# Kernel tuning notes

Measured on AMD Instinct MI355X. Metric: run time of the kernel, lower is better.

Reference implementation:

```python
import jax, jax.numpy as jnp
import numpy as np

N_NODES = 102600
T = 64             # timesteps looped over by the LSTMCell
F_IN = 5           # LSTMCell input size
H = 64             # hidden / GAT channel dim
N_EDGES = 16 * N_NODES


def setup_inputs() -> dict:
    key = jax.random.key(0)
    ks = jax.random.split(key, 12)
    s = 0.1
    return {
        "x": jax.random.normal(ks[0], (N_NODES, T, F_IN), jnp.float32),
        "W_ih": jax.random.normal(ks[1], (4 * H, F_IN), jnp.float32) * s,
        "W_hh": jax.random.normal(ks[2], (4 * H, H), jnp.float32) * s,
        "b_ih": jax.random.normal(ks[3], (4 * H,), jnp.float32) * s,
        "b_hh": jax.random.normal(ks[4], (4 * H,), jnp.float32) * s,
        "gat_w": jax.random.normal(ks[5], (H, H), jnp.float32) * s,
        "att_src": jax.random.normal(ks[6], (H,), jnp.float32) * s,
        "att_dst": jax.random.normal(ks[7], (H,), jnp.float32) * s,
        "gat_bias": jax.random.normal(ks[8], (H,), jnp.float32) * s,
        "fc_w": jax.random.normal(ks[9], (1, H), jnp.float32) * s,
        "fc_b": jax.random.normal(ks[10], (1,), jnp.float32) * s,
        "edge_index": jax.random.randint(ks[11], (2, N_EDGES), 0, N_NODES, dtype=jnp.int64),
    }


def reference(x, W_ih, W_hh, b_ih, b_hh, gat_w, att_src, att_dst, gat_bias, fc_w, fc_b, edge_index):
    N = x.shape[0]
    h0 = jnp.zeros((N, H), x.dtype)
    c0 = jnp.zeros((N, H), x.dtype)

    # --- per-timestep LSTMCell recurrence (torch gate order: i, f, g, o) ---
    def step(carry, xt):
        h, c = carry
        gates = xt @ W_ih.T + b_ih + h @ W_hh.T + b_hh  # [N, 4H]
        i, f, g, o = jnp.split(gates, 4, axis=-1)
        c = jax.nn.sigmoid(f) * c + jax.nn.sigmoid(i) * jnp.tanh(g)
        h = jax.nn.sigmoid(o) * jnp.tanh(c)
        return (h, c), None

    (h, _), _ = jax.lax.scan(step, (h0, c0), jnp.swapaxes(x, 0, 1))  # scan over T

    # --- GATConv(64, 64), heads=1, add_self_loops=True, negative_slope=0.2 ---
    xp = h @ gat_w.T                                   # [N, H] transformed features
    loops = jnp.arange(N, dtype=edge_index.dtype)
    src = jnp.concatenate([edge_index[0], loops])      # message source j
    dst = jnp.concatenate([edge_index[1], loops])      # message target i
    a_src = xp @ att_src                               # [N]
    a_dst = xp @ att_dst                               # [N]
    alpha = jax.nn.leaky_relu(a_src[src] + a_dst[dst], 0.2)  # [E+N]
    # segment softmax over incoming edges per dst node
    amax = jax.ops.segment_max(alpha, dst, num_segments=N)
    ae = jnp.exp(alpha - amax[dst])
    denom = jax.ops.segment_sum(ae, dst, num_segments=N)
    ae = ae / denom[dst]
    out = jax.ops.segment_sum(ae[:, None] * xp[src], dst, num_segments=N) + gat_bias

    # --- fc: Linear(64, 1) + LeakyReLU (default slope 0.01) ---
    return jax.nn.leaky_relu(out @ fc_w.T + fc_b, 0.01)
```

## Files before the change

kernel.cpp:

```cpp
#include <hip/hip_runtime.h>
#include <cstdint>
#include <cstddef>

#define T_STEPS 64
#define F_INP 5
#define LOG2E 1.44269504088896340736f

typedef _Float16 f16x8 __attribute__((ext_vector_type(8)));
typedef float f32x4 __attribute__((ext_vector_type(4)));

__device__ __forceinline__ float leaky(float x, float s){ return x>0.f? x : s*x; }
__device__ __forceinline__ float rcpf(float x){ return __builtin_amdgcn_rcpf(x); }
__device__ __forceinline__ float exp2fast(float x){ return __builtin_amdgcn_exp2f(x); }

__global__ __launch_bounds__(256, 4) void lstm_mfma(
    const float* __restrict__ x, const float* __restrict__ W_ih,
    const float* __restrict__ W_hh, const float* __restrict__ b_ih,
    const float* __restrict__ b_hh, float* __restrict__ h_out, int N)
{
  __shared__ __align__(16) _Float16 Hs0[32][64];
  __shared__ __align__(16) _Float16 Hs1[32][64];
  __shared__ __align__(16) _Float16 Xs0[32][8];
  __shared__ __align__(16) _Float16 Xs1[32][8];
  __shared__ __align__(16) _Float16 Zero8[8];

  const int tid   = threadIdx.x;
  const int lane  = tid & 63;
  const int wq    = tid >> 6;
  const int col16 = lane & 15;
  const int grp   = lane >> 4;
  const int base  = blockIdx.x * 32;

  f16x8 Bh[4][2], Bx[4];
  #pragma unroll
  for (int n=0;n<4;n++){
    const float sc = (n==2) ? 2.f*LOG2E : LOG2E;
    const int gate = n*64 + wq*16 + col16;
    #pragma unroll
    for (int kk=0;kk<2;kk++){
      const float* p = W_hh + gate*64 + kk*32 + grp*8;
      #pragma unroll
      for (int e=0;e<8;e++) Bh[n][kk][e] = (_Float16)(p[e]*sc);
    }
    f16x8 bx = {0,0,0,0,0,0,0,0};
    if (grp==0){
      #pragma unroll
      for (int e=0;e<5;e++) bx[e] = (_Float16)(W_ih[gate*5+e]*sc);
      bx[5] = (_Float16)((b_ih[gate]+b_hh[gate])*sc);
    }
    Bx[n] = bx;
  }

  ((float4*)&Hs0[0][0])[tid] = float4{0.f,0.f,0.f,0.f};
  if (tid==0) ((float4*)Zero8)[0] = float4{0.f,0.f,0.f,0.f};

  const int xnode = tid;
  const bool xown = (tid < 32);
  const int gxn = base + xnode;
  if (xown){
    f16x8 xh = {0,0,0,0,0,0,0,0}; xh[5] = (_Float16)1.f;
    if (gxn < N){
      const float* xp_ = x + (size_t)gxn*(T_STEPS*F_INP);
      #pragma unroll
      for (int j=0;j<F_INP;j++) xh[j] = (_Float16)xp_[j];
    }
    *(f16x8*)&Xs0[xnode][0] = xh;
  }

  const int sw = (col16&7)<<3;
  int roff0[2], roff1[2], xoffm[2], soff[2][4];
  const int j = wq*16 + col16;
  #pragma unroll
  for (int m=0;m<2;m++){
    const int nodeA = 16*m + col16;
    roff0[m] = nodeA*64 + ((grp*8) ^ sw);
    roff1[m] = nodeA*64 + ((32 + grp*8) ^ sw);
    xoffm[m] = nodeA*8;
    #pragma unroll
    for (int r=0;r<4;r++){
      const int node = 16*m + 4*grp + r;
      soff[m][r] = node*64 + (j ^ ((4*(grp&1)+r)<<3));
    }
  }

  float creg[2][4];
  #pragma unroll
  for (int m=0;m<2;m++)
    #pragma unroll
    for (int r=0;r<4;r++) creg[m][r]=0.f;

  __syncthreads();

#define LSTM_STEP(HC, HN, XC, XN, T, LAST) {                                   \
    float xf0=0.f,xf1=0.f,xf2=0.f,xf3=0.f,xf4=0.f;                             \
    const bool xload = (!(LAST)) && xown && (gxn < N);                         \
    if (xload){                                                                \
      const float* xp_ = x + (size_t)gxn*(T_STEPS*F_INP) + ((T)+1)*F_INP;      \
      xf0=xp_[0];xf1=xp_[1];xf2=xp_[2];xf3=xp_[3];xf4=xp_[4];                  \
    }                                                                          \
    _Pragma("unroll")                                                          \
    for (int m=0;m<2;m++){                                                     \
      f16x8 a0 = *(const f16x8*)(&HC[0][0] + roff0[m]);                        \
      f16x8 a1 = *(const f16x8*)(&HC[0][0] + roff1[m]);                        \
      const _Float16* px = (grp==0) ? (&XC[0][0] + xoffm[m]) : Zero8;          \
      f16x8 ax = *(const f16x8*)px;                                            \
      f32x4 z4 = f32x4{0.f,0.f,0.f,0.f};                                       \
      f32x4 ac0=z4, ac1=z4, ac2=z4, ac3=z4;                                    \
      ac0 = __builtin_amdgcn_mfma_f32_16x16x32_f16(a0, Bh[0][0], ac0, 0,0,0);  \
      ac1 = __builtin_amdgcn_mfma_f32_16x16x32_f16(a0, Bh[1][0], ac1, 0,0,0);  \
      ac2 = __builtin_amdgcn_mfma_f32_16x16x32_f16(a0, Bh[2][0], ac2, 0,0,0);  \
      ac3 = __builtin_amdgcn_mfma_f32_16x16x32_f16(a0, Bh[3][0], ac3, 0,0,0);  \
      ac0 = __builtin_amdgcn_mfma_f32_16x16x32_f16(a1, Bh[0][1], ac0, 0,0,0);  \
      ac1 = __builtin_amdgcn_mfma_f32_16x16x32_f16(a1, Bh[1][1], ac1, 0,0,0);  \
      ac2 = __builtin_amdgcn_mfma_f32_16x16x32_f16(a1, Bh[2][1], ac2, 0,0,0);  \
      ac3 = __builtin_amdgcn_mfma_f32_16x16x32_f16(a1, Bh[3][1], ac3, 0,0,0);  \
      ac0 = __builtin_amdgcn_mfma_f32_16x16x32_f16(ax, Bx[0],    ac0, 0,0,0);  \
      ac1 = __builtin_amdgcn_mfma_f32_16x16x32_f16(ax, Bx[1],    ac1, 0,0,0);  \
      ac2 = __builtin_amdgcn_mfma_f32_16x16x32_f16(ax, Bx[2],    ac2, 0,0,0);  \
      ac3 = __builtin_amdgcn_mfma_f32_16x16x32_f16(ax, Bx[3],    ac3, 0,0,0);  \
      _Pragma("unroll")                                                        \
      for (int r=0;r<4;r++){                                                   \
        float e_i = exp2fast(-ac0[r]);                                         \
        float e_f = exp2fast(-ac1[r]);                                         \
        float zg2 = fminf(ac2[r], 60.f);                                       \
        float e_g = exp2fast(zg2);                                             \
        float e_o = exp2fast(-ac3[r]);                                         \
        float Ag = (1.f+e_i)*(1.f+e_g);                                        \
        float Bf = 1.f+e_f;                                                    \
        float rD = rcpf(Ag*Bf);                                                \
        float cn = (creg[m][r]*Ag + (e_g-1.f)*Bf)*rD;                          \
        creg[m][r] = cn;                                                       \
        float c2 = fminf(cn*(2.f*LOG2E), 120.f);                               \
        float e_c = exp2fast(c2);                                              \
        float hv = (e_c-1.f)*rcpf((1.f+e_o)*(1.f+e_c));                        \
        if (LAST){                                                             \
          const int gn = base + 16*m + 4*grp + r;                              \
          if (gn < N) h_out[(size_t)gn*64 + j] = hv;                           \
        } else {                                                               \
          (&HN[0][0])[soff[m][r]] = (_Float16)hv;                              \
        }                                                                      \
      }                                                                        \
    }                                                                          \
    if (!(LAST) && xown){                                                      \
      f16x8 xh = {0,0,0,0,0,0,0,0}; xh[5] = (_Float16)1.f;                     \
      if (xload){                                                              \
        xh[0]=(_Float16)xf0; xh[1]=(_Float16)xf1; xh[2]=(_Float16)xf2;         \
        xh[3]=(_Float16)xf3; xh[4]=(_Float16)xf4;                              \
      }                                                                        \
      *(f16x8*)&XN[xnode][0] = xh;                                             \
    }                                                                          \
  }

  for (int tt=0; tt<T_STEPS/2; ++tt){
    LSTM_STEP(Hs0, Hs1, Xs0, Xs1, 2*tt, false);
    __syncthreads();
    LSTM_STEP(Hs1, Hs0, Xs1, Xs0, 2*tt+1, (tt==T_STEPS/2-1));
    __syncthreads();
  }
#undef LSTM_STEP
}

__global__ void gat_setup(const int* __restrict__ ei,
                          const float* __restrict__ gat_w,
                          const float* __restrict__ att_src,
                          const float* __restrict__ att_dst,
                          const float* __restrict__ fc_w,
                          const float* __restrict__ gat_bias,
                          const float* __restrict__ fc_b,
                          float* __restrict__ vcomb,
                          unsigned* __restrict__ mode)
{
  int j = threadIdx.x;
  unsigned long long nz = __ballot(ei[2*j+1] != 0);
  float bdp = gat_bias[j]*fc_w[j];
  #pragma unroll
  for (int off=32; off; off>>=1) bdp += __shfl_down(bdp, off);
  if (j==0){
    *mode = (nz==0ULL) ? 1u : 0u;
    vcomb[192] = bdp + fc_b[0];
  }
  float va=0.f, vd=0.f, vf=0.f;
  #pragma unroll 8
  for (int k=0;k<64;k++){
    float g = gat_w[k*64+j];
    va += att_src[k]*g;
    vd += att_dst[k]*g;
    vf += fc_w[k]*g;
  }
  vcomb[j]=va; vcomb[64+j]=vd; vcomb[128+j]=vf;
}

__global__ __launch_bounds__(256) void gat_prep(
    const float* __restrict__ h_in, const float* __restrict__ vcomb,
    float* __restrict__ a_src, float* __restrict__ a_dst,
    float* __restrict__ xfv, float* __restrict__ denom,
    float* __restrict__ oacc, int N)
{
  int n = blockIdx.x*256 + threadIdx.x;
  if (n>=N) return;
  const float4* hp = (const float4*)(h_in + (size_t)n*64);
  const float4* va = (const float4*)vcomb;
  const float4* vd = (const float4*)(vcomb+64);
  const float4* vf = (const float4*)(vcomb+128);
  float as=0.f, ad=0.f, xf=0.f;
  #pragma unroll
  for (int q=0;q<16;q++){
    float4 h = hp[q], a = va[q], d = vd[q], f = vf[q];
    as += a.x*h.x + a.y*h.y + a.z*h.z + a.w*h.w;
    ad += d.x*h.x + d.y*h.y + d.z*h.z + d.w*h.w;
    xf += f.x*h.x + f.y*h.y + f.z*h.z + f.w*h.w;
  }
  a_src[n]=as; a_dst[n]=ad; xfv[n]=xf;
  denom[n]=0.f; oacc[n]=0.f;
}

__device__ __forceinline__ void load_edge(const int* ei, unsigned mode,
                                          long long e, long long E,
                                          int& s, int& d)
{
  if (e>=E){ s=d=(int)(e-E); }
  else if (mode){
    const long long* e64 = (const long long*)ei;
    s=(int)e64[e]; d=(int)e64[E+e];
  } else {
    s=ei[e]; d=ei[E+e];
  }
}

__global__ __launch_bounds__(256) void edge_pass(
    const int* __restrict__ ei, const unsigned* __restrict__ mode_p,
    const float* __restrict__ a_src, const float* __restrict__ a_dst,
    const float* __restrict__ xfv,
    float* __restrict__ denom, float* __restrict__ oacc,
    long long E, long long total)
{
  long long e = (long long)blockIdx.x*256 + threadIdx.x;
  if (e>=total) return;
  int s,d;
  load_edge(ei, *mode_p, e, E, s, d);
  float al = leaky(a_src[s]+a_dst[d], 0.2f);
  float ew = __expf(al);
  atomicAdd(&denom[d], ew);
  atomicAdd(&oacc[d], ew * xfv[s]);
}

__global__ __launch_bounds__(256) void finalize(
    const float* __restrict__ oacc, const float* __restrict__ denom,
    const float* __restrict__ vcomb, float* __restrict__ out, int N)
{
  int n = blockIdx.x*256+threadIdx.x;
  if (n>=N) return;
  float v = oacc[n] * rcpf(denom[n]) + vcomb[192];
  out[n] = leaky(v, 0.01f);
}

extern "C" void kernel_launch(void* const* d_in, const int* in_sizes, int n_in,
                              void* d_out, int out_size, void* d_ws, size_t ws_size,
                              hipStream_t stream)
{
  const float* x      = (const float*)d_in[0];
  const float* W_ih   = (const float*)d_in[1];
  const float* W_hh   = (const float*)d_in[2];
  const float* b_ih   = (const float*)d_in[3];
  const float* b_hh   = (const float*)d_in[4];
  const float* gat_w  = (const float*)d_in[5];
  const float* att_s  = (const float*)d_in[6];
  const float* att_d  = (const float*)d_in[7];
  const float* gat_b  = (const float*)d_in[8];
  const float* fc_w   = (const float*)d_in[9];
  const float* fc_b   = (const float*)d_in[10];
  const int*   ei     = (const int*)d_in[11];

  const int N = in_sizes[0]/(T_STEPS*F_INP);
  const long long E = in_sizes[11]/2;
  const long long total = E + N;

  float* ws = (float*)d_ws;
  size_t off = 0;
  float* h_out   = ws + off; off += (size_t)N*64;
  float* a_src   = ws + off; off += (size_t)N;
  float* a_dst   = ws + off; off += (size_t)N;
  float* xfv     = ws + off; off += (size_t)N;
  float* denom   = ws + off; off += (size_t)N;
  float* oacc    = ws + off; off += (size_t)N;
  float* vcomb   = ws + off; off += 256;
  unsigned* mode = (unsigned*)(ws + off); off += 1;

  gat_setup<<<1,64,0,stream>>>(ei, gat_w, att_s, att_d, fc_w, gat_b, fc_b, vcomb, mode);

  lstm_mfma<<<dim3((N+31)/32), dim3(256), 0, stream>>>(
      x, W_ih, W_hh, b_ih, b_hh, h_out, N);

  gat_prep<<<dim3((N+255)/256), dim3(256), 0, stream>>>(
      h_out, vcomb, a_src, a_dst, xfv, denom, oacc, N);

  int eb = (int)((total+255)/256);
  edge_pass<<<dim3(eb), dim3(256), 0, stream>>>(ei, mode, a_src, a_dst, xfv, denom, oacc, E, total);

  finalize<<<dim3((N+255)/256), dim3(256), 0, stream>>>(oacc, denom, vcomb, (float*)d_out, N);
}
```

Measured before the change: 661.4 us.

## Fuse GAT projection into LSTM epilogue and pack src scores

Computes the per-node attention and fc projections directly from the final hidden state held in shared memory at the end of the LSTM kernel. This removes the gat_prep launch and the N x 64 float h_out round trip through global memory. The x loads are now spread across 160 threads with one scalar each, replacing 32 threads loading five values. The MFMA batches for both row halves are issued before the gate math, and a_src and xfv are packed into one float2 so each edge needs one gather for them instead of two. The costs are extra shared memory (a 32x65 float buffer), which may reduce occupancy, and higher register pressure from holding both sets of accumulators.

```diff
diff --git a/kernel.cpp b/kernel.cpp
--- a/kernel.cpp
+++ b/kernel.cpp
@@ -16,13 +16,16 @@
 __global__ __launch_bounds__(256, 4) void lstm_mfma(
     const float* __restrict__ x, const float* __restrict__ W_ih,
     const float* __restrict__ W_hh, const float* __restrict__ b_ih,
-    const float* __restrict__ b_hh, float* __restrict__ h_out, int N)
+    const float* __restrict__ b_hh, const float* __restrict__ vcomb,
+    float2* __restrict__ asx, float* __restrict__ a_dst,
+    float* __restrict__ denom, float* __restrict__ oacc, int N)
 {
   __shared__ __align__(16) _Float16 Hs0[32][64];
   __shared__ __align__(16) _Float16 Hs1[32][64];
   __shared__ __align__(16) _Float16 Xs0[32][8];
   __shared__ __align__(16) _Float16 Xs1[32][8];
   __shared__ __align__(16) _Float16 Zero8[8];
+  __shared__ __align__(16) float    Hf[32][65];
 
   const int tid   = threadIdx.x;
   const int lane  = tid & 63;
@@ -54,17 +57,18 @@
   ((float4*)&Hs0[0][0])[tid] = float4{0.f,0.f,0.f,0.f};
   if (tid==0) ((float4*)Zero8)[0] = float4{0.f,0.f,0.f,0.f};
 
-  const int xnode = tid;
-  const bool xown = (tid < 32);
-  const int gxn = base + xnode;
-  if (xown){
-    f16x8 xh = {0,0,0,0,0,0,0,0}; xh[5] = (_Float16)1.f;
-    if (gxn < N){
-      const float* xp_ = x + (size_t)gxn*(T_STEPS*F_INP);
-      #pragma unroll
-      for (int j=0;j<F_INP;j++) xh[j] = (_Float16)xp_[j];
-    }
-    *(f16x8*)&Xs0[xnode][0] = xh;
+  const int  xn5  = tid/5, xe5 = tid - xn5*5;
+  const bool xact = (tid < 160);
+  const int  gxnode = base + xn5;
+  const bool xlive  = xact && (gxnode < N);
+  const float* xptr = x + (size_t)(xlive ? gxnode : 0)*(T_STEPS*F_INP) + xe5 + F_INP;
+  if (xact){
+    float v0 = xlive ? x[(size_t)gxnode*(T_STEPS*F_INP) + xe5] : 0.f;
+    Xs0[xn5][xe5] = (_Float16)v0;
+  }
+  if (tid < 32){
+    Xs0[tid][5]=(_Float16)1.f; Xs0[tid][6]=(_Float16)0.f; Xs0[tid][7]=(_Float16)0.f;
+    Xs1[tid][5]=(_Float16)1.f; Xs1[tid][6]=(_Float16)0.f; Xs1[tid][7]=(_Float16)0.f;
   }
 
   const int sw = (col16&7)<<3;
@@ -91,13 +95,10 @@
 
   __syncthreads();
 
-#define LSTM_STEP(HC, HN, XC, XN, T, LAST) {                                   \
-    float xf0=0.f,xf1=0.f,xf2=0.f,xf3=0.f,xf4=0.f;                             \
-    const bool xload = (!(LAST)) && xown && (gxn < N);                         \
-    if (xload){                                                                \
-      const float* xp_ = x + (size_t)gxn*(T_STEPS*F_INP) + ((T)+1)*F_INP;      \
-      xf0=xp_[0];xf1=xp_[1];xf2=xp_[2];xf3=xp_[3];xf4=xp_[4];                  \
-    }                                                                          \
+#define LSTM_STEP(HC, HN, XC, XN, XOFF, LAST) {                                \
+    float xval = 0.f;                                                          \
+    if (!(LAST) && xlive) xval = xptr[XOFF];                                   \
+    f32x4 AC0[2], AC1[2], AC2[2], AC3[2];                                      \
     _Pragma("unroll")                                                          \
     for (int m=0;m<2;m++){                                                     \
       f16x8 a0 = *(const f16x8*)(&HC[0][0] + roff0[m]);                        \
@@ -105,59 +106,79 @@
       const _Float16* px = (grp==0) ? (&XC[0][0] + xoffm[m]) : Zero8;          \
       f16x8 ax = *(const f16x8*)px;                                            \
       f32x4 z4 = f32x4{0.f,0.f,0.f,0.f};                                       \
-      f32x4 ac0=z4, ac1=z4, ac2=z4, ac3=z4;                                    \
-      ac0 = __builtin_amdgcn_mfma_f32_16x16x32_f16(a0, Bh[0][0], ac0, 0,0,0);  \
-      ac1 = __builtin_amdgcn_mfma_f32_16x16x32_f16(a0, Bh[1][0], ac1, 0,0,0);  \
-      ac2 = __builtin_amdgcn_mfma_f32_16x16x32_f16(a0, Bh[2][0], ac2, 0,0,0);  \
-      ac3 = __builtin_amdgcn_mfma_f32_16x16x32_f16(a0, Bh[3][0], ac3, 0,0,0);  \
-      ac0 = __builtin_amdgcn_mfma_f32_16x16x32_f16(a1, Bh[0][1], ac0, 0,0,0);  \
-      ac1 = __builtin_amdgcn_mfma_f32_16x16x32_f16(a1, Bh[1][1], ac1, 0,0,0);  \
-      ac2 = __builtin_amdgcn_mfma_f32_16x16x32_f16(a1, Bh[2][1], ac2, 0,0,0);  \
-      ac3 = __builtin_amdgcn_mfma_f32_16x16x32_f16(a1, Bh[3][1], ac3, 0,0,0);  \
-      ac0 = __builtin_amdgcn_mfma_f32_16x16x32_f16(ax, Bx[0],    ac0, 0,0,0);  \
-      ac1 = __builtin_amdgcn_mfma_f32_16x16x32_f16(ax, Bx[1],    ac1, 0,0,0);  \
-      ac2 = __builtin_amdgcn_mfma_f32_16x16x32_f16(ax, Bx[2],    ac2, 0,0,0);  \
-      ac3 = __builtin_amdgcn_mfma_f32_16x16x32_f16(ax, Bx[3],    ac3, 0,0,0);  \
+      f32x4 c0=z4, c1=z4, c2=z4, c3=z4;                                        \
+      c0 = __builtin_amdgcn_mfma_f32_16x16x32_f16(a0, Bh[0][0], c0, 0,0,0);    \
+      c1 = __builtin_amdgcn_mfma_f32_16x16x32_f16(a0, Bh[1][0], c1, 0,0,0);    \
+      c2 = __builtin_amdgcn_mfma_f32_16x16x32_f16(a0, Bh[2][0], c2, 0,0,0);    \
+      c3 = __builtin_amdgcn_mfma_f32_16x16x32_f16(a0, Bh[3][0], c3, 0,0,0);    \
+      c0 = __builtin_amdgcn_mfma_f32_16x16x32_f16(a1, Bh[0][1], c0, 0,0,0);    \
+      c1 = __builtin_amdgcn_mfma_f32_16x16x32_f16(a1, Bh[1][1], c1, 0,0,0);    \
+      c2 = __builtin_amdgcn_mfma_f32_16x16x32_f16(a1, Bh[2][1], c2, 0,0,0);    \
+      c3 = __builtin_amdgcn_mfma_f32_16x16x32_f16(a1, Bh[3][1], c3, 0,0,0);    \
+      c0 = __builtin_amdgcn_mfma_f32_16x16x32_f16(ax, Bx[0],    c0, 0,0,0);    \
+      c1 = __builtin_amdgcn_mfma_f32_16x16x32_f16(ax, Bx[1],    c1, 0,0,0);    \
+      c2 = __builtin_amdgcn_mfma_f32_16x16x32_f16(ax, Bx[2],    c2, 0,0,0);    \
+      c3 = __builtin_amdgcn_mfma_f32_16x16x32_f16(ax, Bx[3],    c3, 0,0,0);    \
+      AC0[m]=c0; AC1[m]=c1; AC2[m]=c2; AC3[m]=c3;                              \
+    }                                                                          \
+    _Pragma("unroll")                                                          \
+    for (int m=0;m<2;m++){                                                     \
       _Pragma("unroll")                                                        \
       for (int r=0;r<4;r++){                                                   \
-        float e_i = exp2fast(-ac0[r]);                                         \
-        float e_f = exp2fast(-ac1[r]);                                         \
-        float zg2 = fminf(ac2[r], 60.f);                                       \
+        float e_i = exp2fast(-AC0[m][r]);                                      \
+        float e_f = exp2fast(-AC1[m][r]);                                      \
+        float zg2 = fminf(AC2[m][r], 60.f);                                    \
         float e_g = exp2fast(zg2);                                             \
-        float e_o = exp2fast(-ac3[r]);                                         \
+        float e_o = exp2fast(-AC3[m][r]);                                      \
         float Ag = (1.f+e_i)*(1.f+e_g);                                        \
         float Bf = 1.f+e_f;                                                    \
         float rD = rcpf(Ag*Bf);                                                \
         float cn = (creg[m][r]*Ag + (e_g-1.f)*Bf)*rD;                          \
         creg[m][r] = cn;                                                       \
-        float c2 = fminf(cn*(2.f*LOG2E), 120.f);                               \
-        float e_c = exp2fast(c2);                                              \
+        float c2v = fminf(cn*(2.f*LOG2E), 120.f);                              \
+        float e_c = exp2fast(c2v);                                             \
         float hv = (e_c-1.f)*rcpf((1.f+e_o)*(1.f+e_c));                        \
         if (LAST){                                                             \
-          const int gn = base + 16*m + 4*grp + r;                              \
-          if (gn < N) h_out[(size_t)gn*64 + j] = hv;                           \
+          Hf[16*m+4*grp+r][j] = hv;                                            \
         } else {                                                               \
           (&HN[0][0])[soff[m][r]] = (_Float16)hv;                              \
         }                                                                      \
       }                                                                        \
     }                                                                          \
-    if (!(LAST) && xown){                                                      \
-      f16x8 xh = {0,0,0,0,0,0,0,0}; xh[5] = (_Float16)1.f;                     \
-      if (xload){                                                              \
-        xh[0]=(_Float16)xf0; xh[1]=(_Float16)xf1; xh[2]=(_Float16)xf2;         \
-        xh[3]=(_Float16)xf3; xh[4]=(_Float16)xf4;                              \
-      }                                                                        \
-      *(f16x8*)&XN[xnode][0] = xh;                                             \
-    }                                                                          \
+    if (!(LAST) && xact) XN[xn5][xe5] = (_Float16)xval;                        \
   }
 
   for (int tt=0; tt<T_STEPS/2; ++tt){
-    LSTM_STEP(Hs0, Hs1, Xs0, Xs1, 2*tt, false);
+    LSTM_STEP(Hs0, Hs1, Xs0, Xs1, 0, false);
     __syncthreads();
-    LSTM_STEP(Hs1, Hs0, Xs1, Xs0, 2*tt+1, (tt==T_STEPS/2-1));
+    LSTM_STEP(Hs1, Hs0, Xs1, Xs0, F_INP, (tt==T_STEPS/2-1));
     __syncthreads();
+    xptr += 2*F_INP;
   }
 #undef LSTM_STEP
+
+  const int en = tid >> 3, es = tid & 7;
+  const int gn2 = base + en;
+  float as=0.f, ad=0.f, xf=0.f;
+  #pragma unroll
+  for (int q=0;q<8;q++){
+    float hv = Hf[en][es*8+q];
+    as = fmaf(hv, vcomb[es*8+q],     as);
+    ad = fmaf(hv, vcomb[64+es*8+q],  ad);
+    xf = fmaf(hv, vcomb[128+es*8+q], xf);
+  }
+  #pragma unroll
+  for (int off=1; off<8; off<<=1){
+    as += __shfl_xor(as, off);
+    ad += __shfl_xor(ad, off);
+    xf += __shfl_xor(xf, off);
+  }
+  if (es==0 && gn2 < N){
+    asx[gn2]   = float2{as, xf};
+    a_dst[gn2] = ad;
+    denom[gn2] = 0.f;
+    oacc[gn2]  = 0.f;
+  }
 }
 
 __global__ void gat_setup(const int* __restrict__ ei,
@@ -190,30 +211,6 @@
   vcomb[j]=va; vcomb[64+j]=vd; vcomb[128+j]=vf;
 }
 
-__global__ __launch_bounds__(256) void gat_prep(
-    const float* __restrict__ h_in, const float* __restrict__ vcomb,
-    float* __restrict__ a_src, float* __restrict__ a_dst,
-    float* __restrict__ xfv, float* __restrict__ denom,
-    float* __restrict__ oacc, int N)
-{
-  int n = blockIdx.x*256 + threadIdx.x;
-  if (n>=N) return;
-  const float4* hp = (const float4*)(h_in + (size_t)n*64);
-  const float4* va = (const float4*)vcomb;
-  const float4* vd = (const float4*)(vcomb+64);
-  const float4* vf = (const float4*)(vcomb+128);
-  float as=0.f, ad=0.f, xf=0.f;
-  #pragma unroll
-  for (int q=0;q<16;q++){
-    float4 h = hp[q], a = va[q], d = vd[q], f = vf[q];
-    as += a.x*h.x + a.y*h.y + a.z*h.z + a.w*h.w;
-    ad += d.x*h.x + d.y*h.y + d.z*h.z + d.w*h.w;
-    xf += f.x*h.x + f.y*h.y + f.z*h.z + f.w*h.w;
-  }
-  a_src[n]=as; a_dst[n]=ad; xfv[n]=xf;
-  denom[n]=0.f; oacc[n]=0.f;
-}
-
 __device__ __forceinline__ void load_edge(const int* ei, unsigned mode,
                                           long long e, long long E,
                                           int& s, int& d)
@@ -229,8 +226,7 @@
 
 __global__ __launch_bounds__(256) void edge_pass(
     const int* __restrict__ ei, const unsigned* __restrict__ mode_p,
-    const float* __restrict__ a_src, const float* __restrict__ a_dst,
-    const float* __restrict__ xfv,
+    const float2* __restrict__ asx, const float* __restrict__ a_dst,
     float* __restrict__ denom, float* __restrict__ oacc,
     long long E, long long total)
 {
@@ -238,10 +234,11 @@
   if (e>=total) return;
   int s,d;
   load_edge(ei, *mode_p, e, E, s, d);
-  float al = leaky(a_src[s]+a_dst[d], 0.2f);
+  float2 sv = asx[s];
+  float al = leaky(sv.x + a_dst[d], 0.2f);
   float ew = __expf(al);
   atomicAdd(&denom[d], ew);
-  atomicAdd(&oacc[d], ew * xfv[s]);
+  atomicAdd(&oacc[d], ew * sv.y);
 }
 
 __global__ __launch_bounds__(256) void finalize(
@@ -277,10 +274,8 @@
 
   float* ws = (float*)d_ws;
   size_t off = 0;
-  float* h_out   = ws + off; off += (size_t)N*64;
-  float* a_src   = ws + off; off += (size_t)N;
+  float2* asx    = (float2*)(ws + off); off += (size_t)2*N;
   float* a_dst   = ws + off; off += (size_t)N;
-  float* xfv     = ws + off; off += (size_t)N;
   float* denom   = ws + off; off += (size_t)N;
   float* oacc    = ws + off; off += (size_t)N;
   float* vcomb   = ws + off; off += 256;
@@ -289,13 +284,10 @@
   gat_setup<<<1,64,0,stream>>>(ei, gat_w, att_s, att_d, fc_w, gat_b, fc_b, vcomb, mode);
 
   lstm_mfma<<<dim3((N+31)/32), dim3(256), 0, stream>>>(
-      x, W_ih, W_hh, b_ih, b_hh, h_out, N);
-
-  gat_prep<<<dim3((N+255)/256), dim3(256), 0, stream>>>(
-      h_out, vcomb, a_src, a_dst, xfv, denom, oacc, N);
+      x, W_ih, W_hh, b_ih, b_hh, vcomb, asx, a_dst, denom, oacc, N);
 
   int eb = (int)((total+255)/256);
-  edge_pass<<<dim3(eb), dim3(256), 0, stream>>>(ei, mode, a_src, a_dst, xfv, denom, oacc, E, total);
+  edge_pass<<<dim3(eb), dim3(256), 0, stream>>>(ei, mode, asx, a_dst, denom, oacc, E, total);
 
   finalize<<<dim3((N+255)/256), dim3(256), 0, stream>>>(oacc, denom, vcomb, (float*)d_out, N);
 }
```

Result: no change. 650.6 us (-1.6%).
